# Performance work log

Measured on AMD Instinct MI355X. Metric: run time of the kernel, lower is better.

Reference implementation:

```python
import jax, jax.numpy as jnp
import numpy as np

D = 64          # internal token dim (patch_encoder output)
E = 4           # num_experts
HID = 256       # expert hidden dim
NCLS = 10       # classifier output (hardcoded in source)


def gelu(x):
    return jax.nn.gelu(x, approximate=False)  # torch nn.GELU default = exact erf


def setup_inputs() -> dict:
    key = jax.random.key(0)
    ks = jax.random.split(key, 16)
    B, S, IN = 128, 1024, 192
    sc = lambda k, sh, fan: (jax.random.normal(k, sh, jnp.float32) / np.sqrt(fan))
    return {
        "x": jax.random.normal(ks[0], (B, S, IN), jnp.float32),
        # patch encoder: Linear(IN,64) -> GELU -> Linear(64,D)
        "pe_w1": sc(ks[1], (IN, 64), IN), "pe_b1": jnp.zeros((64,), jnp.float32),
        "pe_w2": sc(ks[2], (64, D), 64),  "pe_b2": jnp.zeros((D,), jnp.float32),
        # gate: Linear(D, E)
        "gate_w": sc(ks[3], (D, E), D), "gate_b": jnp.zeros((E,), jnp.float32),
        # experts: per-expert MLP D -> HID -> D
        "ew1": sc(ks[4], (E, D, HID), D), "eb1": jnp.zeros((E, HID), jnp.float32),
        "ew2": sc(ks[5], (E, HID, D), HID), "eb2": jnp.zeros((E, D), jnp.float32),
        # classifier: LayerNorm(D) -> Linear(D,D) -> GELU -> Linear(D,10)
        "ln_g": jnp.ones((D,), jnp.float32), "ln_b": jnp.zeros((D,), jnp.float32),
        "cl_w1": sc(ks[6], (D, D), D), "cl_b1": jnp.zeros((D,), jnp.float32),
        "cl_w2": sc(ks[7], (D, NCLS), D), "cl_b2": jnp.zeros((NCLS,), jnp.float32),
    }


def reference(x, pe_w1, pe_b1, pe_w2, pe_b2, gate_w, gate_b,
              ew1, eb1, ew2, eb2, ln_g, ln_b, cl_w1, cl_b1, cl_w2, cl_b2):
    # patch encoder: [B,S,IN] -> [B,S,D]
    h = gelu(x @ pe_w1 + pe_b1) @ pe_w2 + pe_b2

    # top-1 gating
    gate_logits = h @ gate_w + gate_b                      # [B,S,E]
    probs = jax.nn.softmax(gate_logits, axis=-1)
    top1 = jnp.argmax(probs, axis=-1)                      # [B,S] int
    onehot = jax.nn.one_hot(top1, E, dtype=h.dtype)        # [B,S,E] dispatch mask
    gate = jnp.sum(probs * onehot, axis=-1)                # [B,S] top-1 gate value

    # expert MLPs computed densely, combined by one-hot mask (same math as dispatch)
    eh = gelu(jnp.einsum('bsd,edh->bseh', h, ew1) + eb1)   # [B,S,E,HID]
    eo = jnp.einsum('bseh,ehd->bsed', eh, ew2) + eb2       # [B,S,E,D]
    moe_out = jnp.einsum('bsed,bse->bsd', eo, onehot) * gate[..., None]

    # switch-style load-balance aux loss: E * sum_e f_e * P_e
    f = jnp.mean(onehot, axis=(0, 1))                      # fraction routed per expert
    p = jnp.mean(probs, axis=(0, 1))                       # mean gate prob per expert
    aux_loss = E * jnp.sum(f * p)

    # mean pool over sequence, then classifier
    z = jnp.mean(moe_out, axis=1)                          # [B,D]
    mu = jnp.mean(z, axis=-1, keepdims=True)
    var = jnp.var(z, axis=-1, keepdims=True)
    zn = (z - mu) * jax.lax.rsqrt(var + 1e-5) * ln_g + ln_b
    y = gelu(zn @ cl_w1 + cl_b1) @ cl_w2 + cl_b2           # [B,10]
    return (y, aux_loss)
```

## Files before the change

kernel.cpp:

```cpp
#include <hip/hip_runtime.h>
#include <hip/hip_bf16.h>
#include <math.h>

typedef unsigned int  u32;
typedef unsigned short u16;
typedef unsigned long long u64;

using bf16x8  = __attribute__((ext_vector_type(8))) __bf16;
using float4v = __attribute__((ext_vector_type(4))) float;

#define MFMA16(a,b,c) __builtin_amdgcn_mfma_f32_16x16x32_bf16(a,b,c,0,0,0)

#define W1P_OFF   0u
#define W2P_OFF   24576u
#define GWP_OFF   40960u
#define E1P_OFF   43008u
#define E2P_OFF   174080u
#define ZF_OFF    305152u
#define CNTF_OFF  337920u
#define PSUMF_OFF 337984u
#define FAST_WS_BYTES 338048u

#define Z_OFF    0u
#define CNT_OFF  32768u
#define PSUM_OFF 32832u

__device__ inline u16 f2bf(float f){
  union { float f; u32 u; } v; v.f = f;
  u32 r = v.u + 0x7fffu + ((v.u >> 16) & 1u);
  return (u16)(r >> 16);
}
__device__ inline u32 pk2(float a, float b){
  union { __hip_bfloat162 h2; u32 u; } v;
  v.h2 = __float22bfloat162_rn(make_float2(a, b));
  return v.u;
}

__device__ inline float geluf(float x){
  float u = fabsf(x) * 0.70710678118654752f;
  float t = __builtin_amdgcn_rcpf(1.0f + 0.3275911f * u);
  float poly = t*(0.254829592f + t*(-0.284496736f +
               t*(1.421413741f + t*(-1.453152027f + t*1.061405429f))));
  float er = 1.0f - poly * __expf(-u*u);
  return 0.5f * x * (1.0f + copysignf(er, x));
}

__global__ __launch_bounds__(256) void k0_pack(
    const float* __restrict__ w1, const float* __restrict__ w2, const float* __restrict__ gw,
    const float* __restrict__ e1, const float* __restrict__ e2,
    u16* w1p, u16* w2p, u16* gwp, u16* e1p, u16* e2p,
    float* z, u32* cnt, float* psum)
{
  int d = blockIdx.x*256 + threadIdx.x;
  int lane = d & 63, col = lane & 15, q = lane >> 4;
  if (d < 1536){
    int tile = d >> 6, kc = tile >> 2, mt = tile & 3;
    int m = mt*16 + col, k0 = kc*32 + q*8;
    uint4 v;
    v.x = pk2(w1[(k0+0)*64+m], w1[(k0+1)*64+m]);
    v.y = pk2(w1[(k0+2)*64+m], w1[(k0+3)*64+m]);
    v.z = pk2(w1[(k0+4)*64+m], w1[(k0+5)*64+m]);
    v.w = pk2(w1[(k0+6)*64+m], w1[(k0+7)*64+m]);
    *(uint4*)(w1p + d*8) = v; return;
  }
  d -= 1536;
  if (d < 512){
    int tile = d >> 6, kc = tile >> 2, mt = tile & 3;
    int m = mt*16 + col, k0 = kc*32 + q*8;
    uint4 v;
    v.x = pk2(w2[(k0+0)*64+m], w2[(k0+1)*64+m]);
    v.y = pk2(w2[(k0+2)*64+m], w2[(k0+3)*64+m]);
    v.z = pk2(w2[(k0+4)*64+m], w2[(k0+5)*64+m]);
    v.w = pk2(w2[(k0+6)*64+m], w2[(k0+7)*64+m]);
    *(uint4*)(w2p + d*8) = v; return;
  }
  d -= 512;
  if (d < 128){
    int kc = d >> 6, k0 = kc*32 + q*8;
    uint4 v = {0u,0u,0u,0u};
    if (col < 4){
      v.x = pk2(gw[(k0+0)*4+col], gw[(k0+1)*4+col]);
      v.y = pk2(gw[(k0+2)*4+col], gw[(k0+3)*4+col]);
      v.z = pk2(gw[(k0+4)*4+col], gw[(k0+5)*4+col]);
      v.w = pk2(gw[(k0+6)*4+col], gw[(k0+7)*4+col]);
    }
    *(uint4*)(gwp + d*8) = v; return;
  }
  d -= 128;
  if (d < 8192){
    int e = d >> 11, t2 = d & 2047;
    int tile = t2 >> 6, kc = tile >> 4, mt = tile & 15;
    int m = mt*16 + col, k0 = kc*32 + q*8;
    const float* s = e1 + e*16384;
    uint4 v;
    v.x = pk2(s[(k0+0)*256+m], s[(k0+1)*256+m]);
    v.y = pk2(s[(k0+2)*256+m], s[(k0+3)*256+m]);
    v.z = pk2(s[(k0+4)*256+m], s[(k0+5)*256+m]);
    v.w = pk2(s[(k0+6)*256+m], s[(k0+7)*256+m]);
    *(uint4*)(e1p + d*8) = v; return;
  }
  d -= 8192;
  if (d < 8192){
    int e = d >> 11, t2 = d & 2047;
    int tile = t2 >> 6, kc = tile >> 2, mt = tile & 3;
    int m = mt*16 + col, k0 = kc*32 + q*8;
    const float* s = e2 + e*16384;
    uint4 v;
    v.x = pk2(s[(k0+0)*64+m], s[(k0+1)*64+m]);
    v.y = pk2(s[(k0+2)*64+m], s[(k0+3)*64+m]);
    v.z = pk2(s[(k0+4)*64+m], s[(k0+5)*64+m]);
    v.w = pk2(s[(k0+6)*64+m], s[(k0+7)*64+m]);
    *(uint4*)(e2p + d*8) = v; return;
  }
  d -= 8192;
  if (d < 8192){ z[d] = 0.f; return; }
  d -= 8192;
  if (d < 4){ cnt[d] = 0u; return; }
  d -= 4;
  if (d < 4){ psum[d] = 0.f; return; }
}

__global__ __launch_bounds__(256) void kMain(
    const float* __restrict__ x,
    const float* __restrict__ b1, const float* __restrict__ b2, const float* __restrict__ gb,
    const u16* __restrict__ w1p, const u16* __restrict__ w2p, const u16* __restrict__ gwp,
    const u16* __restrict__ e1p, const u16* __restrict__ e2p,
    const float* __restrict__ eb1, const float* __restrict__ eb2,
    float* __restrict__ z, u32* __restrict__ cnt, float* __restrict__ psum)
{
  __shared__ char wreg[13312];
  __shared__ char hl[9216];
  __shared__ int   be_s[64];
  __shared__ float gv_s[64];
  __shared__ int   sperm[64];
  __shared__ int   se_s[64];
  __shared__ float sg_s[64];
  __shared__ float lgp[4];
  __shared__ u32   lgc[4];

  const int tid  = threadIdx.x;
  const int lane = tid & 63, wave = tid >> 6;
  const int col  = lane & 15, quad = lane >> 4;
  const int tok0 = blockIdx.x * 64;
  const int t    = wave*16 + col;
  if (tid < 4){ lgp[tid] = 0.f; lgc[tid] = 0u; }

  char* wr = wreg + wave*3328;

  const float* xw = x + (size_t)(tok0 + wave*16)*192;
  bf16x8 bx[6];
  for (int h = 0; h < 2; ++h){
    for (int it = 0; it < 3; ++it){
      int task = it*64 + lane;
      int tr = task / 12, c = task % 12;
      const float* src = xw + tr*192 + h*96 + c*8;
      float4 f0 = *(const float4*)(src);
      float4 f1 = *(const float4*)(src + 4);
      uint4 v;
      v.x = pk2(f0.x,f0.y); v.y = pk2(f0.z,f0.w);
      v.z = pk2(f1.x,f1.y); v.w = pk2(f1.z,f1.w);
      *(uint4*)(wr + tr*208 + c*16) = v;
    }
    for (int kc = 0; kc < 3; ++kc)
      bx[h*3 + kc] = *(const bf16x8*)(wr + col*208 + (4*kc + quad)*16);
  }

  char* h1t = wr;
  for (int mt = 0; mt < 4; ++mt){
    float4v acc = {0.f,0.f,0.f,0.f};
    for (int kc = 0; kc < 6; ++kc){
      bf16x8 a = *(const bf16x8*)(w1p + ((kc*4 + mt)*64 + lane)*8);
      acc = MFMA16(a, bx[kc], acc);
    }
    int j0 = mt*16 + quad*4;
    float4 bb = *(const float4*)(b1 + j0);
    uint2 w; w.x = pk2(geluf(acc[0]+bb.x), geluf(acc[1]+bb.y));
             w.y = pk2(geluf(acc[2]+bb.z), geluf(acc[3]+bb.w));
    *(uint2*)(h1t + col*144 + mt*32 + quad*8) = w;
  }

  {
    bf16x8 bh1[2];
    for (int kc = 0; kc < 2; ++kc)
      bh1[kc] = *(const bf16x8*)(h1t + col*144 + (4*kc+quad)*16);
    for (int mt = 0; mt < 4; ++mt){
      float4v acc = {0.f,0.f,0.f,0.f};
      for (int kc = 0; kc < 2; ++kc){
        bf16x8 a = *(const bf16x8*)(w2p + ((kc*4 + mt)*64 + lane)*8);
        acc = MFMA16(a, bh1[kc], acc);
      }
      int j0 = mt*16 + quad*4;
      float4 bb = *(const float4*)(b2 + j0);
      uint2 w; w.x = pk2(acc[0]+bb.x, acc[1]+bb.y);
               w.y = pk2(acc[2]+bb.z, acc[3]+bb.w);
      *(uint2*)(hl + t*144 + mt*32 + quad*8) = w;
    }
  }

  float p0=0.f,p1=0.f,p2=0.f,p3=0.f; int be=0;
  {
    bf16x8 bh[2];
    for (int kc = 0; kc < 2; ++kc)
      bh[kc] = *(const bf16x8*)(hl + t*144 + (4*kc+quad)*16);
    float4v ag = {0.f,0.f,0.f,0.f};
    for (int kc = 0; kc < 2; ++kc){
      bf16x8 a = *(const bf16x8*)(gwp + (kc*64 + lane)*8);
      ag = MFMA16(a, bh[kc], ag);
    }
    if (quad == 0){
      float l0 = ag[0]+gb[0], l1 = ag[1]+gb[1], l2 = ag[2]+gb[2], l3 = ag[3]+gb[3];
      float mx = fmaxf(fmaxf(l0,l1), fmaxf(l2,l3));
      float x0 = __expf(l0-mx), x1 = __expf(l1-mx), x2 = __expf(l2-mx), x3 = __expf(l3-mx);
      float inv = __builtin_amdgcn_rcpf(x0+x1+x2+x3);
      p0 = x0*inv; p1 = x1*inv; p2 = x2*inv; p3 = x3*inv;
      float bv = l0; be = 0;
      if (l1 > bv){ bv = l1; be = 1; }
      if (l2 > bv){ bv = l2; be = 2; }
      if (l3 > bv){ bv = l3; be = 3; }
      be_s[t] = be;
      gv_s[t] = (be==0) ? p0 : (be==1) ? p1 : (be==2) ? p2 : p3;
    }
  }
  __syncthreads();
  if (quad == 0){
    atomicAdd(&lgp[0], p0); atomicAdd(&lgp[1], p1);
    atomicAdd(&lgp[2], p2); atomicAdd(&lgp[3], p3);
    atomicAdd(&lgc[be], 1u);
  }

  if (tid < 64){
    int e = be_s[tid];
    u64 m0 = __ballot(e==0), m1 = __ballot(e==1), m2 = __ballot(e==2), m3 = __ballot(e==3);
    int c0 = __popcll(m0), c1 = __popcll(m1), c2 = __popcll(m2);
    int base = (e==0) ? 0 : (e==1) ? c0 : (e==2) ? c0+c1 : c0+c1+c2;
    u64 me = (e==0) ? m0 : (e==1) ? m1 : (e==2) ? m2 : m3;
    int pos = base + __popcll(me & ((1ull<<tid)-1ull));
    sperm[pos] = tid; se_s[pos] = e; sg_s[pos] = gv_s[tid];
  }
  __syncthreads();

  const int slice = wave*16;
  const int tt    = sperm[slice + col];
  const int myE   = se_s[slice + col];
  const float myG = sg_s[slice + col];
  const int e_lo  = se_s[slice], e_hi = se_s[slice + 15];
  char* hbt = wr;

  bf16x8 bhp[2];
  for (int kc = 0; kc < 2; ++kc)
    bhp[kc] = *(const bf16x8*)(hl + tt*144 + (4*kc+quad)*16);

  float oacc[16];
  for (int i = 0; i < 16; ++i) oacc[i] = 0.f;

  for (int e = e_lo; e <= e_hi; ++e){
    const u16* W1 = e1p + e*16384;
    const u16* W2 = e2p + e*16384;
    float4v accE[4];
    for (int mt = 0; mt < 4; ++mt) accE[mt] = (float4v){0.f,0.f,0.f,0.f};
    for (int p = 0; p < 4; ++p){
      for (int mt2 = 0; mt2 < 4; ++mt2){
        float4v acc = {0.f,0.f,0.f,0.f};
        for (int kc = 0; kc < 2; ++kc){
          bf16x8 a = *(const bf16x8*)(W1 + ((kc*16 + p*4 + mt2)*64 + lane)*8);
          acc = MFMA16(a, bhp[kc], acc);
        }
        int j0 = p*64 + mt2*16 + quad*4;
        float4 bb = *(const float4*)(eb1 + e*256 + j0);
        uint2 w; w.x = pk2(geluf(acc[0]+bb.x), geluf(acc[1]+bb.y));
                 w.y = pk2(geluf(acc[2]+bb.z), geluf(acc[3]+bb.w));
        *(uint2*)(hbt + col*144 + mt2*32 + quad*8) = w;
      }
      bf16x8 bq0 = *(const bf16x8*)(hbt + col*144 + quad*16);
      bf16x8 bq1 = *(const bf16x8*)(hbt + col*144 + (4+quad)*16);
      for (int mt = 0; mt < 4; ++mt){
        bf16x8 a0 = *(const bf16x8*)(W2 + (((p*2+0)*4 + mt)*64 + lane)*8);
        bf16x8 a1 = *(const bf16x8*)(W2 + (((p*2+1)*4 + mt)*64 + lane)*8);
        accE[mt] = MFMA16(a0, bq0, accE[mt]);
        accE[mt] = MFMA16(a1, bq1, accE[mt]);
      }
    }
    float wgt = (myE == e) ? myG : 0.f;
    for (int mt = 0; mt < 4; ++mt){
      float4 bb = *(const float4*)(eb2 + e*64 + mt*16 + quad*4);
      oacc[mt*4+0] += (accE[mt][0] + bb.x) * wgt;
      oacc[mt*4+1] += (accE[mt][1] + bb.y) * wgt;
      oacc[mt*4+2] += (accE[mt][2] + bb.z) * wgt;
      oacc[mt*4+3] += (accE[mt][3] + bb.w) * wgt;
    }
  }

  for (int m = 1; m < 16; m <<= 1)
    for (int i = 0; i < 16; ++i)
      oacc[i] += __shfl_xor(oacc[i], m, 64);
  if (col == 0){
    float* pw = (float*)wr;
    for (int mt = 0; mt < 4; ++mt)
      for (int r = 0; r < 4; ++r)
        pw[mt*16 + quad*4 + r] = oacc[mt*4 + r];
  }
  __syncthreads();
  int b = blockIdx.x >> 4;
  if (tid < 64){
    float s = *(const float*)(wreg + tid*4)        + *(const float*)(wreg + 3328 + tid*4)
            + *(const float*)(wreg + 6656 + tid*4) + *(const float*)(wreg + 9984 + tid*4);
    atomicAdd(&z[b*64 + tid], s);
  }
  if (tid < 4){ atomicAdd(&cnt[tid], lgc[tid]); atomicAdd(&psum[tid], lgp[tid]); }
}

__global__ __launch_bounds__(64) void kFinal(
    const float* __restrict__ z, const u32* __restrict__ cnt, const float* __restrict__ psum,
    const float* __restrict__ ln_g, const float* __restrict__ ln_b,
    const float* __restrict__ cw1, const float* __restrict__ cb1,
    const float* __restrict__ cw2, const float* __restrict__ cb2,
    float* __restrict__ out)
{
  __shared__ float z_l[64], zn_l[64], c1_l[64], red[2];
  int tid = threadIdx.x, b = blockIdx.x;
  z_l[tid] = z[b*64 + tid] * (1.0f/1024.0f);
  __syncthreads();
  if (tid == 0){
    float mu = 0.f; for (int i=0;i<64;++i) mu += z_l[i]; mu *= (1.f/64.f);
    float vv = 0.f; for (int i=0;i<64;++i){ float d=z_l[i]-mu; vv += d*d; } vv *= (1.f/64.f);
    red[0]=mu; red[1]=1.0f/sqrtf(vv+1e-5f);
  }
  __syncthreads();
  zn_l[tid] = (z_l[tid]-red[0])*red[1]*ln_g[tid] + ln_b[tid];
  __syncthreads();
  float a1 = cb1[tid];
  for (int k=0;k<64;++k) a1 += zn_l[k]*cw1[k*64+tid];
  c1_l[tid] = geluf(a1);
  __syncthreads();
  if (tid < 10){
    float y = cb2[tid];
    for (int k=0;k<64;++k) y += c1_l[k]*cw2[k*10+tid];
    out[b*10+tid] = y;
  }
  if (b == 0 && tid == 0){
    float aux = 0.f;
    for (int e=0;e<4;++e) aux += (float)cnt[e]*psum[e];
    out[1280] = 4.0f*aux/(131072.0f*131072.0f);
  }
}

__global__ __launch_bounds__(256) void kInitF(float* z, u32* cnt, float* psum){
  int i = blockIdx.x*256 + threadIdx.x;
  if (i < 8192) z[i] = 0.f;
  if (i < 4){ cnt[i] = 0u; psum[i] = 0.f; }
}

__global__ __launch_bounds__(256) void kFusedF(
    const float* __restrict__ x,
    const float* __restrict__ w1, const float* __restrict__ b1,
    const float* __restrict__ w2, const float* __restrict__ b2,
    const float* __restrict__ gw, const float* __restrict__ gb,
    const float* __restrict__ e1, const float* __restrict__ eb1,
    const float* __restrict__ e2, const float* __restrict__ eb2,
    float* __restrict__ z, u32* __restrict__ cnt, float* __restrict__ psum)
{
  __shared__ float xs[4][192];
  __shared__ float h1s[4][64];
  __shared__ float hs[4][64];
  __shared__ float hid[4][256];
  __shared__ float lg[4][4];
  __shared__ int   be_s[4];
  __shared__ float gv_s[4];
  __shared__ float lgp[4];
  __shared__ u32   lgc[4];
  const int tid  = threadIdx.x;
  const int w    = tid >> 6, lane = tid & 63;
  const int tok  = blockIdx.x*4 + w;
  if (tid < 4){ lgp[tid] = 0.f; lgc[tid] = 0u; }
  for (int r = 0; r < 3; ++r)
    xs[w][lane + 64*r] = x[(size_t)tok*192 + lane + 64*r];
  __syncthreads();
  float a = b1[lane];
  for (int k = 0; k < 192; ++k) a += xs[w][k]*w1[k*64 + lane];
  h1s[w][lane] = geluf(a);
  __syncthreads();
  float h = b2[lane];
  for (int k = 0; k < 64; ++k) h += h1s[w][k]*w2[k*64 + lane];
  hs[w][lane] = h;
  __syncthreads();
  if (lane < 4){
    float l = gb[lane];
    for (int k = 0; k < 64; ++k) l += hs[w][k]*gw[k*4 + lane];
    lg[w][lane] = l;
  }
  __syncthreads();
  if (lane == 0){
    float l0=lg[w][0], l1=lg[w][1], l2=lg[w][2], l3=lg[w][3];
    float mx = fmaxf(fmaxf(l0,l1),fmaxf(l2,l3));
    float x0=expf(l0-mx), x1=expf(l1-mx), x2=expf(l2-mx), x3=expf(l3-mx);
    float inv = 1.f/(x0+x1+x2+x3);
    float p0=x0*inv, p1=x1*inv, p2=x2*inv, p3=x3*inv;
    int be=0; float bv=l0;
    if (l1>bv){bv=l1;be=1;}
    if (l2>bv){bv=l2;be=2;}
    if (l3>bv){bv=l3;be=3;}
    be_s[w]=be;
    gv_s[w]=(be==0)?p0:(be==1)?p1:(be==2)?p2:p3;
    atomicAdd(&lgp[0],p0); atomicAdd(&lgp[1],p1);
    atomicAdd(&lgp[2],p2); atomicAdd(&lgp[3],p3);
    atomicAdd(&lgc[be],1u);
  }
  __syncthreads();
  const int e    = be_s[w];
  const float gv = gv_s[w];
  const float* W1 = e1 + e*16384;
  const float* W2 = e2 + e*16384;
  for (int q = 0; q < 4; ++q){
    int j = q*64 + lane;
    float s = eb1[e*256 + j];
    for (int k = 0; k < 64; ++k) s += hs[w][k]*W1[k*256 + j];
    hid[w][j] = geluf(s);
  }
  __syncthreads();
  float o = eb2[e*64 + lane];
  for (int j = 0; j < 256; ++j) o += hid[w][j]*W2[j*64 + lane];
  int b = tok >> 10;
  atomicAdd(&z[b*64 + lane], o*gv);
  __syncthreads();
  if (tid < 4){ atomicAdd(&cnt[tid], lgc[tid]); atomicAdd(&psum[tid], lgp[tid]); }
}

extern "C" void kernel_launch(void* const* d_in, const int* in_sizes, int n_in,
                              void* d_out, int out_size, void* d_ws, size_t ws_size,
                              hipStream_t stream)
{
  const float* x    = (const float*)d_in[0];
  const float* pw1  = (const float*)d_in[1];
  const float* pb1  = (const float*)d_in[2];
  const float* pw2  = (const float*)d_in[3];
  const float* pb2  = (const float*)d_in[4];
  const float* gw   = (const float*)d_in[5];
  const float* gb   = (const float*)d_in[6];
  const float* ew1  = (const float*)d_in[7];
  const float* eb1  = (const float*)d_in[8];
  const float* ew2  = (const float*)d_in[9];
  const float* eb2  = (const float*)d_in[10];
  const float* lng  = (const float*)d_in[11];
  const float* lnb  = (const float*)d_in[12];
  const float* cw1  = (const float*)d_in[13];
  const float* cb1  = (const float*)d_in[14];
  const float* cw2  = (const float*)d_in[15];
  const float* cb2  = (const float*)d_in[16];
  char* ws  = (char*)d_ws;
  float* out = (float*)d_out;

  if (ws_size >= FAST_WS_BYTES){
    u16*  w1p  = (u16*)(ws + W1P_OFF);
    u16*  w2p  = (u16*)(ws + W2P_OFF);
    u16*  gwp  = (u16*)(ws + GWP_OFF);
    u16*  e1p  = (u16*)(ws + E1P_OFF);
    u16*  e2p  = (u16*)(ws + E2P_OFF);
    float* z    = (float*)(ws + ZF_OFF);
    u32*  cnt  = (u32*)(ws + CNTF_OFF);
    float* psum = (float*)(ws + PSUMF_OFF);
    k0_pack<<<105, 256, 0, stream>>>(pw1, pw2, gw, ew1, ew2,
                                     w1p, w2p, gwp, e1p, e2p, z, cnt, psum);
    kMain <<<2048, 256, 0, stream>>>(x, pb1, pb2, gb, w1p, w2p, gwp, e1p, e2p,
                                     eb1, eb2, z, cnt, psum);
    kFinal<<<128, 64, 0, stream>>>(z, cnt, psum, lng, lnb, cw1, cb1, cw2, cb2, out);
  } else {
    float* z    = (float*)(ws + Z_OFF);
    u32*   cnt  = (u32*)(ws + CNT_OFF);
    float* psum = (float*)(ws + PSUM_OFF);
    kInitF <<<32,    256, 0, stream>>>(z, cnt, psum);
    kFusedF<<<32768, 256, 0, stream>>>(x, pw1, pb1, pw2, pb2, gw, gb,
                                       ew1, eb1, ew2, eb2, z, cnt, psum);
    kFinal <<<128,   64,  0, stream>>>(z, cnt, psum, lng, lnb, cw1, cb1, cw2, cb2, out);
  }
}
```

Baseline: 278.4 us.

## Process 256 tokens per block so each expert weight fragment feeds four token groups

```diff
diff --git a/kernel.cpp b/kernel.cpp
--- a/kernel.cpp
+++ b/kernel.cpp
@@ -35,7 +35,6 @@
   v.h2 = __float22bfloat162_rn(make_float2(a, b));
   return v.u;
 }
-
 __device__ inline float geluf(float x){
   float u = fabsf(x) * 0.70710678118654752f;
   float t = __builtin_amdgcn_rcpf(1.0f + 0.3275911f * u);
@@ -120,7 +119,7 @@
   if (d < 4){ psum[d] = 0.f; return; }
 }
 
-__global__ __launch_bounds__(256) void kMain(
+__global__ __launch_bounds__(256, 2) void kMain(
     const float* __restrict__ x,
     const float* __restrict__ b1, const float* __restrict__ b2, const float* __restrict__ gb,
     const u16* __restrict__ w1p, const u16* __restrict__ w2p, const u16* __restrict__ gwp,
@@ -128,165 +127,187 @@
     const float* __restrict__ eb1, const float* __restrict__ eb2,
     float* __restrict__ z, u32* __restrict__ cnt, float* __restrict__ psum)
 {
+  __shared__ char hl[36864];
   __shared__ char wreg[13312];
-  __shared__ char hl[9216];
-  __shared__ int   be_s[64];
-  __shared__ float gv_s[64];
-  __shared__ int   sperm[64];
-  __shared__ int   se_s[64];
-  __shared__ float sg_s[64];
+  __shared__ int   be_s[256];
+  __shared__ float gv_s[256];
+  __shared__ int   sperm[256];
+  __shared__ int   se_s[256];
+  __shared__ float sg_s[256];
+  __shared__ int   cmat[4][4];
   __shared__ float lgp[4];
   __shared__ u32   lgc[4];
 
   const int tid  = threadIdx.x;
   const int lane = tid & 63, wave = tid >> 6;
   const int col  = lane & 15, quad = lane >> 4;
-  const int tok0 = blockIdx.x * 64;
-  const int t    = wave*16 + col;
+  const int tok0 = blockIdx.x * 256;
   if (tid < 4){ lgp[tid] = 0.f; lgc[tid] = 0u; }
 
   char* wr = wreg + wave*3328;
-
-  const float* xw = x + (size_t)(tok0 + wave*16)*192;
-  bf16x8 bx[6];
-  for (int h = 0; h < 2; ++h){
-    for (int it = 0; it < 3; ++it){
-      int task = it*64 + lane;
-      int tr = task / 12, c = task % 12;
-      const float* src = xw + tr*192 + h*96 + c*8;
-      float4 f0 = *(const float4*)(src);
-      float4 f1 = *(const float4*)(src + 4);
-      uint4 v;
-      v.x = pk2(f0.x,f0.y); v.y = pk2(f0.z,f0.w);
-      v.z = pk2(f1.x,f1.y); v.w = pk2(f1.z,f1.w);
-      *(uint4*)(wr + tr*208 + c*16) = v;
-    }
-    for (int kc = 0; kc < 3; ++kc)
-      bx[h*3 + kc] = *(const bf16x8*)(wr + col*208 + (4*kc + quad)*16);
-  }
-
-  char* h1t = wr;
-  for (int mt = 0; mt < 4; ++mt){
-    float4v acc = {0.f,0.f,0.f,0.f};
-    for (int kc = 0; kc < 6; ++kc){
-      bf16x8 a = *(const bf16x8*)(w1p + ((kc*4 + mt)*64 + lane)*8);
-      acc = MFMA16(a, bx[kc], acc);
-    }
-    int j0 = mt*16 + quad*4;
-    float4 bb = *(const float4*)(b1 + j0);
-    uint2 w; w.x = pk2(geluf(acc[0]+bb.x), geluf(acc[1]+bb.y));
-             w.y = pk2(geluf(acc[2]+bb.z), geluf(acc[3]+bb.w));
-    *(uint2*)(h1t + col*144 + mt*32 + quad*8) = w;
-  }
-
-  {
+  float gp0=0.f, gp1=0.f, gp2=0.f, gp3=0.f;
+  int beg[4] = {0,0,0,0};
+
+  for (int g = 0; g < 4; ++g){
+    const int trow = wave*64 + g*16;
+    const float* xw = x + (size_t)(tok0 + trow)*192;
+    bf16x8 bx[6];
+    for (int h = 0; h < 2; ++h){
+      for (int it = 0; it < 3; ++it){
+        int task = it*64 + lane;
+        int tr = task / 12, c = task % 12;
+        const float* src = xw + tr*192 + h*96 + c*8;
+        float4 f0 = *(const float4*)(src);
+        float4 f1 = *(const float4*)(src + 4);
+        uint4 v;
+        v.x = pk2(f0.x,f0.y); v.y = pk2(f0.z,f0.w);
+        v.z = pk2(f1.x,f1.y); v.w = pk2(f1.z,f1.w);
+        *(uint4*)(wr + tr*208 + c*16) = v;
+      }
+      for (int kc = 0; kc < 3; ++kc)
+        bx[h*3+kc] = *(const bf16x8*)(wr + col*208 + (4*kc+quad)*16);
+    }
+    char* h1t = wr;
+    for (int mt = 0; mt < 4; ++mt){
+      float4v acc = {0.f,0.f,0.f,0.f};
+      for (int kc = 0; kc < 6; ++kc){
+        bf16x8 a = *(const bf16x8*)(w1p + ((kc*4+mt)*64 + lane)*8);
+        acc = MFMA16(a, bx[kc], acc);
+      }
+      int j0 = mt*16 + quad*4;
+      float4 bb = *(const float4*)(b1 + j0);
+      uint2 wv; wv.x = pk2(geluf(acc[0]+bb.x), geluf(acc[1]+bb.y));
+                wv.y = pk2(geluf(acc[2]+bb.z), geluf(acc[3]+bb.w));
+      *(uint2*)(h1t + col*144 + mt*32 + quad*8) = wv;
+    }
     bf16x8 bh1[2];
     for (int kc = 0; kc < 2; ++kc)
       bh1[kc] = *(const bf16x8*)(h1t + col*144 + (4*kc+quad)*16);
+    const int hrow = trow + col;
     for (int mt = 0; mt < 4; ++mt){
       float4v acc = {0.f,0.f,0.f,0.f};
       for (int kc = 0; kc < 2; ++kc){
-        bf16x8 a = *(const bf16x8*)(w2p + ((kc*4 + mt)*64 + lane)*8);
+        bf16x8 a = *(const bf16x8*)(w2p + ((kc*4+mt)*64 + lane)*8);
         acc = MFMA16(a, bh1[kc], acc);
       }
       int j0 = mt*16 + quad*4;
       float4 bb = *(const float4*)(b2 + j0);
-      uint2 w; w.x = pk2(acc[0]+bb.x, acc[1]+bb.y);
-               w.y = pk2(acc[2]+bb.z, acc[3]+bb.w);
-      *(uint2*)(hl + t*144 + mt*32 + quad*8) = w;
-    }
-  }
-
-  float p0=0.f,p1=0.f,p2=0.f,p3=0.f; int be=0;
-  {
+      uint2 wv; wv.x = pk2(acc[0]+bb.x, acc[1]+bb.y);
+                wv.y = pk2(acc[2]+bb.z, acc[3]+bb.w);
+      *(uint2*)(hl + hrow*144 + mt*32 + quad*8) = wv;
+    }
     bf16x8 bh[2];
     for (int kc = 0; kc < 2; ++kc)
-      bh[kc] = *(const bf16x8*)(hl + t*144 + (4*kc+quad)*16);
+      bh[kc] = *(const bf16x8*)(hl + hrow*144 + (4*kc+quad)*16);
     float4v ag = {0.f,0.f,0.f,0.f};
     for (int kc = 0; kc < 2; ++kc){
-      bf16x8 a = *(const bf16x8*)(gwp + (kc*64 + lane)*8);
+      bf16x8 a = *(const bf16x8*)(gwp + (kc*64+lane)*8);
       ag = MFMA16(a, bh[kc], ag);
     }
     if (quad == 0){
-      float l0 = ag[0]+gb[0], l1 = ag[1]+gb[1], l2 = ag[2]+gb[2], l3 = ag[3]+gb[3];
-      float mx = fmaxf(fmaxf(l0,l1), fmaxf(l2,l3));
-      float x0 = __expf(l0-mx), x1 = __expf(l1-mx), x2 = __expf(l2-mx), x3 = __expf(l3-mx);
+      float l0=ag[0]+gb[0], l1=ag[1]+gb[1], l2=ag[2]+gb[2], l3=ag[3]+gb[3];
+      float mx = fmaxf(fmaxf(l0,l1),fmaxf(l2,l3));
+      float x0=__expf(l0-mx), x1=__expf(l1-mx), x2=__expf(l2-mx), x3=__expf(l3-mx);
       float inv = __builtin_amdgcn_rcpf(x0+x1+x2+x3);
-      p0 = x0*inv; p1 = x1*inv; p2 = x2*inv; p3 = x3*inv;
-      float bv = l0; be = 0;
-      if (l1 > bv){ bv = l1; be = 1; }
-      if (l2 > bv){ bv = l2; be = 2; }
-      if (l3 > bv){ bv = l3; be = 3; }
-      be_s[t] = be;
-      gv_s[t] = (be==0) ? p0 : (be==1) ? p1 : (be==2) ? p2 : p3;
-    }
-  }
-  __syncthreads();
+      float p0=x0*inv,p1=x1*inv,p2=x2*inv,p3=x3*inv;
+      int be=0; float bv=l0;
+      if (l1>bv){bv=l1;be=1;}
+      if (l2>bv){bv=l2;be=2;}
+      if (l3>bv){bv=l3;be=3;}
+      be_s[hrow] = be;
+      gv_s[hrow] = (be==0)?p0:(be==1)?p1:(be==2)?p2:p3;
+      gp0+=p0; gp1+=p1; gp2+=p2; gp3+=p3;
+      beg[g]=be;
+    }
+  }
+  __syncthreads();
+
   if (quad == 0){
-    atomicAdd(&lgp[0], p0); atomicAdd(&lgp[1], p1);
-    atomicAdd(&lgp[2], p2); atomicAdd(&lgp[3], p3);
-    atomicAdd(&lgc[be], 1u);
-  }
-
-  if (tid < 64){
+    atomicAdd(&lgp[0],gp0); atomicAdd(&lgp[1],gp1);
+    atomicAdd(&lgp[2],gp2); atomicAdd(&lgp[3],gp3);
+    for (int g = 0; g < 4; ++g) atomicAdd(&lgc[beg[g]],1u);
+  }
+
+  {
     int e = be_s[tid];
-    u64 m0 = __ballot(e==0), m1 = __ballot(e==1), m2 = __ballot(e==2), m3 = __ballot(e==3);
-    int c0 = __popcll(m0), c1 = __popcll(m1), c2 = __popcll(m2);
-    int base = (e==0) ? 0 : (e==1) ? c0 : (e==2) ? c0+c1 : c0+c1+c2;
-    u64 me = (e==0) ? m0 : (e==1) ? m1 : (e==2) ? m2 : m3;
-    int pos = base + __popcll(me & ((1ull<<tid)-1ull));
+    u64 m0=__ballot(e==0), m1=__ballot(e==1), m2=__ballot(e==2), m3=__ballot(e==3);
+    if (lane < 4){
+      u64 mm = (lane==0)?m0:(lane==1)?m1:(lane==2)?m2:m3;
+      cmat[wave][lane] = __popcll(mm);
+    }
+    u64 me = (e==0)?m0:(e==1)?m1:(e==2)?m2:m3;
+    int r = __popcll(me & ((1ull<<lane)-1ull));
+    __syncthreads();
+    int base = 0;
+    for (int ee = 0; ee < 4; ++ee)
+      for (int w2_ = 0; w2_ < 4; ++w2_)
+        if (ee < e || (ee == e && w2_ < wave)) base += cmat[w2_][ee];
+    int pos = base + r;
     sperm[pos] = tid; se_s[pos] = e; sg_s[pos] = gv_s[tid];
   }
   __syncthreads();
 
-  const int slice = wave*16;
-  const int tt    = sperm[slice + col];
-  const int myE   = se_s[slice + col];
-  const float myG = sg_s[slice + col];
-  const int e_lo  = se_s[slice], e_hi = se_s[slice + 15];
-  char* hbt = wr;
-
-  bf16x8 bhp[2];
-  for (int kc = 0; kc < 2; ++kc)
-    bhp[kc] = *(const bf16x8*)(hl + tt*144 + (4*kc+quad)*16);
-
+  const int sbase = wave*64;
+  int myE[4]; float myG[4]; bf16x8 bhp[4][2];
+  for (int g = 0; g < 4; ++g){
+    int sp = sbase + g*16 + col;
+    int tt = sperm[sp];
+    myE[g] = se_s[sp]; myG[g] = sg_s[sp];
+    for (int kc = 0; kc < 2; ++kc)
+      bhp[g][kc] = *(const bf16x8*)(hl + tt*144 + (4*kc+quad)*16);
+  }
+  const int e_lo = se_s[sbase], e_hi = se_s[sbase+63];
+  __syncthreads();
+
+  char* hb = hl + wave*9216;
   float oacc[16];
   for (int i = 0; i < 16; ++i) oacc[i] = 0.f;
 
   for (int e = e_lo; e <= e_hi; ++e){
     const u16* W1 = e1p + e*16384;
     const u16* W2 = e2p + e*16384;
-    float4v accE[4];
-    for (int mt = 0; mt < 4; ++mt) accE[mt] = (float4v){0.f,0.f,0.f,0.f};
+    float4v accD[4][4];
+    for (int mt = 0; mt < 4; ++mt)
+      for (int g = 0; g < 4; ++g)
+        accD[mt][g] = (float4v){0.f,0.f,0.f,0.f};
     for (int p = 0; p < 4; ++p){
       for (int mt2 = 0; mt2 < 4; ++mt2){
-        float4v acc = {0.f,0.f,0.f,0.f};
-        for (int kc = 0; kc < 2; ++kc){
-          bf16x8 a = *(const bf16x8*)(W1 + ((kc*16 + p*4 + mt2)*64 + lane)*8);
-          acc = MFMA16(a, bhp[kc], acc);
-        }
+        bf16x8 a0 = *(const bf16x8*)(W1 + ((      p*4+mt2)*64 + lane)*8);
+        bf16x8 a1 = *(const bf16x8*)(W1 + ((16 +  p*4+mt2)*64 + lane)*8);
         int j0 = p*64 + mt2*16 + quad*4;
         float4 bb = *(const float4*)(eb1 + e*256 + j0);
-        uint2 w; w.x = pk2(geluf(acc[0]+bb.x), geluf(acc[1]+bb.y));
-                 w.y = pk2(geluf(acc[2]+bb.z), geluf(acc[3]+bb.w));
-        *(uint2*)(hbt + col*144 + mt2*32 + quad*8) = w;
-      }
-      bf16x8 bq0 = *(const bf16x8*)(hbt + col*144 + quad*16);
-      bf16x8 bq1 = *(const bf16x8*)(hbt + col*144 + (4+quad)*16);
+        for (int g = 0; g < 4; ++g){
+          float4v acc = {0.f,0.f,0.f,0.f};
+          acc = MFMA16(a0, bhp[g][0], acc);
+          acc = MFMA16(a1, bhp[g][1], acc);
+          uint2 wv; wv.x = pk2(geluf(acc[0]+bb.x), geluf(acc[1]+bb.y));
+                    wv.y = pk2(geluf(acc[2]+bb.z), geluf(acc[3]+bb.w));
+          *(uint2*)(hb + g*2304 + col*144 + mt2*32 + quad*8) = wv;
+        }
+      }
+      bf16x8 bq[4][2];
+      for (int g = 0; g < 4; ++g){
+        bq[g][0] = *(const bf16x8*)(hb + g*2304 + col*144 + quad*16);
+        bq[g][1] = *(const bf16x8*)(hb + g*2304 + col*144 + (4+quad)*16);
+      }
       for (int mt = 0; mt < 4; ++mt){
-        bf16x8 a0 = *(const bf16x8*)(W2 + (((p*2+0)*4 + mt)*64 + lane)*8);
-        bf16x8 a1 = *(const bf16x8*)(W2 + (((p*2+1)*4 + mt)*64 + lane)*8);
-        accE[mt] = MFMA16(a0, bq0, accE[mt]);
-        accE[mt] = MFMA16(a1, bq1, accE[mt]);
-      }
-    }
-    float wgt = (myE == e) ? myG : 0.f;
+        bf16x8 a0 = *(const bf16x8*)(W2 + (((p*2+0)*4+mt)*64 + lane)*8);
+        bf16x8 a1 = *(const bf16x8*)(W2 + (((p*2+1)*4+mt)*64 + lane)*8);
+        for (int g = 0; g < 4; ++g){
+          accD[mt][g] = MFMA16(a0, bq[g][0], accD[mt][g]);
+          accD[mt][g] = MFMA16(a1, bq[g][1], accD[mt][g]);
+        }
+      }
+    }
     for (int mt = 0; mt < 4; ++mt){
       float4 bb = *(const float4*)(eb2 + e*64 + mt*16 + quad*4);
-      oacc[mt*4+0] += (accE[mt][0] + bb.x) * wgt;
-      oacc[mt*4+1] += (accE[mt][1] + bb.y) * wgt;
-      oacc[mt*4+2] += (accE[mt][2] + bb.z) * wgt;
-      oacc[mt*4+3] += (accE[mt][3] + bb.w) * wgt;
+      for (int g = 0; g < 4; ++g){
+        float wgt = (myE[g]==e) ? myG[g] : 0.f;
+        oacc[mt*4+0] += (accD[mt][g][0]+bb.x)*wgt;
+        oacc[mt*4+1] += (accD[mt][g][1]+bb.y)*wgt;
+        oacc[mt*4+2] += (accD[mt][g][2]+bb.z)*wgt;
+        oacc[mt*4+3] += (accD[mt][g][3]+bb.w)*wgt;
+      }
     }
   }
 
@@ -300,7 +321,7 @@
         pw[mt*16 + quad*4 + r] = oacc[mt*4 + r];
   }
   __syncthreads();
-  int b = blockIdx.x >> 4;
+  int b = blockIdx.x >> 2;
   if (tid < 64){
     float s = *(const float*)(wreg + tid*4)        + *(const float*)(wreg + 3328 + tid*4)
             + *(const float*)(wreg + 6656 + tid*4) + *(const float*)(wreg + 9984 + tid*4);
@@ -460,8 +481,8 @@
     float* psum = (float*)(ws + PSUMF_OFF);
     k0_pack<<<105, 256, 0, stream>>>(pw1, pw2, gw, ew1, ew2,
                                      w1p, w2p, gwp, e1p, e2p, z, cnt, psum);
-    kMain <<<2048, 256, 0, stream>>>(x, pb1, pb2, gb, w1p, w2p, gwp, e1p, e2p,
-                                     eb1, eb2, z, cnt, psum);
+    kMain <<<512, 256, 0, stream>>>(x, pb1, pb2, gb, w1p, w2p, gwp, e1p, e2p,
+                                    eb1, eb2, z, cnt, psum);
     kFinal<<<128, 64, 0, stream>>>(z, cnt, psum, lng, lnb, cw1, cb1, cw2, cb2, out);
   } else {
     float* z    = (float*)(ws + Z_OFF);
```

New measurement: 241.3 us. -13.3%, faster.
